# Optimization experiments

Hardware: AMD Instinct MI355X
Metric: run time of the kernel (lower is better)

## Reference

```python
import jax, jax.numpy as jnp
import numpy as np

T, B, IN, H = 512, 64, 512, 1024

def setup_inputs() -> dict:
    key = jax.random.key(0)
    ks = jax.random.split(key, 9)
    s_w = 1.0 / np.sqrt(H + IN)  # torch Linear default init scale
    inp = {"x": jax.random.normal(ks[0], (T, B, IN), dtype=jnp.float32)}
    for name, k in zip(["f", "i", "c", "o"], ks[1:5]):
        inp["W" + name] = jax.random.uniform(k, (H, H + IN), dtype=jnp.float32, minval=-s_w, maxval=s_w)
    for name, k in zip(["f", "i", "c", "o"], ks[5:9]):
        inp["b" + name] = jax.random.uniform(k, (H,), dtype=jnp.float32, minval=-s_w, maxval=s_w)
    return inp

def reference(x, Wf, bf, Wi, bi, Wc, bc, Wo, bo):
    # x: [T, B, IN]; initial h, c are zeros (h=None, c=None path in torch code)
    Bsz = x.shape[1]
    h0 = jnp.zeros((Bsz, H), dtype=x.dtype)
    c0 = jnp.zeros((Bsz, H), dtype=x.dtype)

    def step(carry, x_t):
        h, c = carry
        hx = jnp.concatenate([h, x_t], axis=-1)          # [B, H+IN]
        f = jax.nn.sigmoid(hx @ Wf.T + bf)
        i = jax.nn.sigmoid(hx @ Wi.T + bi)
        c_hat = jnp.tanh(hx @ Wc.T + bc)
        new_c = f * c + i * c_hat
        o = jax.nn.sigmoid(hx @ Wo.T + bo)
        new_h = o * jnp.tanh(new_c)
        return (new_h, new_c), new_h

    _, hs = jax.lax.scan(step, (h0, c0), x)              # hs: [T, B, H]
    return hs
```

## Files before the change

kernel.cpp:

```cpp
#include <hip/hip_runtime.h>
#include <hip/hip_bf16.h>
#include <stdint.h>

#define T_STEPS 512
#define BATCH   64
#define IN_DIM  512
#define H_DIM   1024
#define KDIM    1536
#define NWG     256
#define NTHREADS 256

#define WLDS_OFF 0
#define WLDS_BYTES (24*4*64*16)
#define HA_OFF   98304
#define XA_OFF   131072
#define SMZ_OFF  147456
#define LDS_TOTAL 151616

#define WS_SYNC 0
#define WS_HB   32768
#define WS_XB   294912
#define WS_WPK  33849344

typedef float  f32x4  __attribute__((ext_vector_type(4)));
typedef short  short8 __attribute__((ext_vector_type(8)));
typedef int    int4v  __attribute__((ext_vector_type(4)));
typedef __bf16 bf16x8 __attribute__((ext_vector_type(8)));

__device__ __forceinline__ short f2bf(float f) {
    union { float f; unsigned u; } x; x.f = f;
    unsigned r = (x.u + 0x7fffu + ((x.u >> 16) & 1u)) >> 16;
    return (short)r;
}
__device__ __forceinline__ f32x4 bmfma(short8 a, short8 b, f32x4 c) {
    return __builtin_amdgcn_mfma_f32_16x16x32_bf16(
        __builtin_bit_cast(bf16x8, a), __builtin_bit_cast(bf16x8, b), c, 0, 0, 0);
}

__global__ __launch_bounds__(256) void pack_w_kernel(const float* __restrict__ W,
                                                     short* __restrict__ Wpk, int g) {
    int e = blockIdx.x * 256 + threadIdx.x;
    int j = e / KDIM, k = e - j * KDIM;
    int cb = j >> 4, n = j & 15;
    int ks = k >> 5, grp = (k & 31) >> 3, u = k & 7;
    size_t dst = (((size_t)(cb * 48 + ks) * 4 + g) * 64 + grp * 16 + n) * 8 + u;
    Wpk[dst] = f2bf(W[e]);
}

__global__ __launch_bounds__(256) void xconv_kernel(const float* __restrict__ x,
                                                    short* __restrict__ xb) {
    int e = blockIdx.x * 256 + threadIdx.x;
    int t = e >> 12, rem = e & 4095;
    int brow = rem >> 6, chunk = rem & 63;
    const float* src = x + ((size_t)t * 64 + brow) * IN_DIM + chunk * 8;
    f32x4 v0 = *reinterpret_cast<const f32x4*>(src);
    f32x4 v1 = *reinterpret_cast<const f32x4*>(src + 4);
    short8 o;
    #pragma unroll
    for (int u = 0; u < 4; ++u) { o[u] = f2bf(v0[u]); o[4 + u] = f2bf(v1[u]); }
    int bt = brow >> 4, row = brow & 15, ks = chunk >> 2, grp = chunk & 3;
    size_t dst = (((size_t)t * 4 + bt) * 1024 + ks * 64 + grp * 16 + row) * 8;
    *reinterpret_cast<short8*>(xb + dst) = o;
}

__global__ __launch_bounds__(256) void init_state_kernel(int* sync, int* hb_i) {
    int e = blockIdx.x * 256 + threadIdx.x;
    if (e < 8192) sync[e] = 0;
    if (e < 65536) hb_i[e] = 0;
}

extern "C" __global__ void __launch_bounds__(NTHREADS, 1)
lstm_persistent(const short* __restrict__ Wpk, const short* __restrict__ xb,
                short* __restrict__ hb, float* __restrict__ out,
                const float* __restrict__ bf_, const float* __restrict__ bi_,
                const float* __restrict__ bc_, const float* __restrict__ bo_,
                int* __restrict__ sync)
{
    extern __shared__ char lds[];
    short* Wlds = (short*)(lds + WLDS_OFF);
    short* hA   = (short*)(lds + HA_OFF);
    short* xA   = (short*)(lds + XA_OFF);
    float* smZ  = (float*)(lds + SMZ_OFF);

    const int tid = threadIdx.x, w = tid >> 6, lane = tid & 63;
    const int wg = blockIdx.x;
    const int bt = wg >> 6, cb = wg & 63;
    const int r = lane & 15, hi = lane >> 4;

    const int erow = tid >> 4, ecol = tid & 15;
    const int col_g = cb * 16 + ecol;
    const int row_g = bt * 16 + erow;
    const float bfv = bf_[col_g], biv = bi_[col_g], bcv = bc_[col_g], bov = bo_[col_g];
    float creg = 0.f;

    const int chunkP = col_g >> 3, uP = col_g & 7;
    const int ksP = chunkP >> 2, grpP = chunkP & 3;
    const int pub_off = (ksP * 64 + grpP * 16 + erow) * 8 + uP;

    int* mybarr = sync + bt * 64;

    const short* wgrp = Wpk + (size_t)cb * (48 * 4 * 64 * 8);
    #pragma unroll
    for (int q = 0; q < 24; ++q) {
        int sl = q * 256 + tid;
        *reinterpret_cast<short8*>(Wlds + sl * 8) =
            *reinterpret_cast<const short8*>(wgrp + (size_t)sl * 8);
    }
    const short* wstream = wgrp + (((size_t)24 * 4 + w) * 64 + lane) * 8;

    {
        const short* xtile = xb + ((size_t)0 * 4 + bt) * (1024 * 8);
        #pragma unroll
        for (int q = 0; q < 4; ++q) {
            int sl = q * 256 + tid;
            *reinterpret_cast<short8*>(&xA[sl * 8]) =
                *reinterpret_cast<const short8*>(xtile + (size_t)sl * 8);
        }
    }

    for (int t = 0; t < T_STEPS; ++t) {
        if (t > 0) {
            if (tid == 0) {
                while (__hip_atomic_load(mybarr, __ATOMIC_RELAXED, __HIP_MEMORY_SCOPE_AGENT) < 64 * t)
                    __builtin_amdgcn_s_sleep(1);
            }
        }
        __syncthreads();

        const short* htile = hb + (size_t)(t & 1) * (BATCH * H_DIM) + bt * 16384;
        unsigned long long hlo[8], hhi[8];
        #pragma unroll
        for (int q = 0; q < 8; ++q) {
            const unsigned long long* src = reinterpret_cast<const unsigned long long*>(
                htile + (size_t)(q * 256 + tid) * 8);
            hlo[q] = __hip_atomic_load(src,     __ATOMIC_RELAXED, __HIP_MEMORY_SCOPE_AGENT);
            hhi[q] = __hip_atomic_load(src + 1, __ATOMIC_RELAXED, __HIP_MEMORY_SCOPE_AGENT);
        }
        __builtin_amdgcn_sched_barrier(0);

        f32x4 acc[4];
        #pragma unroll
        for (int c = 0; c < 4; ++c) acc[c] = (f32x4){0.f, 0.f, 0.f, 0.f};
        #pragma unroll
        for (int ksx = 0; ksx < 16; ++ksx) {
            short8 a = *reinterpret_cast<const short8*>(&xA[(ksx * 64 + lane) * 8]);
            short8 b = *reinterpret_cast<const short8*>(wstream + (size_t)(8 + ksx) * 2048);
            acc[ksx & 3] = bmfma(a, b, acc[ksx & 3]);
        }
        __builtin_amdgcn_sched_barrier(0);

        #pragma unroll
        for (int q = 0; q < 8; ++q) {
            unsigned long long tmp[2] = {hlo[q], hhi[q]};
            *reinterpret_cast<int4v*>(&hA[(q * 256 + tid) * 8]) =
                *reinterpret_cast<const int4v*>(tmp);
        }
        __syncthreads();

        #pragma unroll
        for (int ks = 0; ks < 24; ++ks) {
            short8 a = *reinterpret_cast<const short8*>(&hA[(ks * 64 + lane) * 8]);
            short8 b = *reinterpret_cast<const short8*>(Wlds + ((size_t)(ks * 4 + w) * 64 + lane) * 8);
            acc[ks & 3] = bmfma(a, b, acc[ks & 3]);
        }
        #pragma unroll
        for (int ks = 24; ks < 32; ++ks) {
            short8 a = *reinterpret_cast<const short8*>(&hA[(ks * 64 + lane) * 8]);
            short8 b = *reinterpret_cast<const short8*>(wstream + (size_t)(ks - 24) * 2048);
            acc[ks & 3] = bmfma(a, b, acc[ks & 3]);
        }

        f32x4 z4 = (acc[0] + acc[1]) + (acc[2] + acc[3]);
        #pragma unroll
        for (int i = 0; i < 4; ++i)
            smZ[(hi * 4 + i) * 65 + w * 16 + r] = z4[i];
        __syncthreads();

        float zf = smZ[erow * 65 + ecol]      + bfv;
        float zi = smZ[erow * 65 + 16 + ecol] + biv;
        float zc = smZ[erow * 65 + 32 + ecol] + bcv;
        float zo = smZ[erow * 65 + 48 + ecol] + bov;
        float fg  = 1.f / (1.f + __expf(-zf));
        float ig  = 1.f / (1.f + __expf(-zi));
        float cg_ = 2.f / (1.f + __expf(-2.f * zc)) - 1.f;
        float og  = 1.f / (1.f + __expf(-zo));
        creg = fg * creg + ig * cg_;
        float nh = og * (2.f / (1.f + __expf(-2.f * creg)) - 1.f);

        unsigned mybits = (unsigned)(unsigned short)f2bf(nh);
        unsigned pbits  = __shfl_xor(mybits, 1);
        short* hnext_tile = hb + (size_t)((t + 1) & 1) * (BATCH * H_DIM) + bt * 16384;
        if ((tid & 1) == 0) {
            unsigned val = mybits | (pbits << 16);
            __hip_atomic_store(reinterpret_cast<unsigned*>(hnext_tile + pub_off),
                               val, __ATOMIC_RELAXED, __HIP_MEMORY_SCOPE_AGENT);
        }

        __syncthreads();
        if (tid == 0)
            __hip_atomic_fetch_add(mybarr, 1, __ATOMIC_RELAXED, __HIP_MEMORY_SCOPE_AGENT);

        out[(size_t)t * (BATCH * H_DIM) + (size_t)row_g * H_DIM + col_g] = nh;
        if (t + 1 < T_STEPS) {
            const short* xtile = xb + ((size_t)(t + 1) * 4 + bt) * (1024 * 8);
            #pragma unroll
            for (int q = 0; q < 4; ++q) {
                int sl = q * 256 + tid;
                *reinterpret_cast<short8*>(&xA[sl * 8]) =
                    *reinterpret_cast<const short8*>(xtile + (size_t)sl * 8);
            }
        }
    }
}

extern "C" void kernel_launch(void* const* d_in, const int* in_sizes, int n_in,
                              void* d_out, int out_size, void* d_ws, size_t ws_size,
                              hipStream_t stream) {
    const float* x   = (const float*)d_in[0];
    const float* Wf  = (const float*)d_in[1];
    const float* Wi  = (const float*)d_in[2];
    const float* Wc  = (const float*)d_in[3];
    const float* Wo  = (const float*)d_in[4];
    const float* bf_ = (const float*)d_in[5];
    const float* bi_ = (const float*)d_in[6];
    const float* bc_ = (const float*)d_in[7];
    const float* bo_ = (const float*)d_in[8];
    float* out = (float*)d_out;

    char*  ws    = (char*)d_ws;
    int*   syncp = (int*)(ws + WS_SYNC);
    short* hbuf  = (short*)(ws + WS_HB);
    short* xb    = (short*)(ws + WS_XB);
    short* Wpk   = (short*)(ws + WS_WPK);

    hipFuncSetAttribute((const void*)lstm_persistent,
                        hipFuncAttributeMaxDynamicSharedMemorySize, LDS_TOTAL);

    const float* Ws[4] = {Wf, Wi, Wc, Wo};
    for (int g = 0; g < 4; ++g)
        pack_w_kernel<<<(H_DIM * KDIM) / 256, 256, 0, stream>>>(Ws[g], Wpk, g);
    xconv_kernel<<<(T_STEPS * BATCH * IN_DIM) / (256 * 8), 256, 0, stream>>>(x, xb);
    init_state_kernel<<<256, 256, 0, stream>>>(syncp, (int*)hbuf);

    const short* Wpk_c = Wpk; const short* xb_c = xb;
    void* args[] = {(void*)&Wpk_c, (void*)&xb_c, (void*)&hbuf, (void*)&out,
                    (void*)&bf_, (void*)&bi_, (void*)&bc_, (void*)&bo_, (void*)&syncp};
    hipLaunchCooperativeKernel((const void*)lstm_persistent, dim3(NWG), dim3(NTHREADS),
                               args, LDS_TOTAL, stream);
}
```

Before: 1.558 ms.

## Split K dimension across two wave groups with 512 threads per workgroup

Doubles the workgroup to 8 waves and splits the K-reduction of each gate tile between two 4-wave groups. Group 0 uses the LDS-resident weights for h[0:16] and x[0:8], while group 1 streams the remaining weight chunks from global memory. The partial accumulators are combined through a new LDS buffer before the gate nonlinearities. This halves the serial MFMA chain per wave on the critical recurrent path, at the cost of an extra LDS reduction and barrier and an uneven balance between LDS-fed and global-fed groups.

```diff
diff --git a/kernel.cpp b/kernel.cpp
--- a/kernel.cpp
+++ b/kernel.cpp
@@ -8,14 +8,15 @@
 #define H_DIM   1024
 #define KDIM    1536
 #define NWG     256
-#define NTHREADS 256
+#define NTHREADS 512
 
 #define WLDS_OFF 0
 #define WLDS_BYTES (24*4*64*16)
 #define HA_OFF   98304
 #define XA_OFF   131072
-#define SMZ_OFF  147456
-#define LDS_TOTAL 151616
+#define SMP_OFF  147456
+#define SMZ_OFF  151552
+#define LDS_TOTAL 155712
 
 #define WS_SYNC 0
 #define WS_HB   32768
@@ -80,14 +81,17 @@
     short* Wlds = (short*)(lds + WLDS_OFF);
     short* hA   = (short*)(lds + HA_OFF);
     short* xA   = (short*)(lds + XA_OFF);
+    float* smP  = (float*)(lds + SMP_OFF);
     float* smZ  = (float*)(lds + SMZ_OFF);
 
     const int tid = threadIdx.x, w = tid >> 6, lane = tid & 63;
     const int wg = blockIdx.x;
     const int bt = wg >> 6, cb = wg & 63;
     const int r = lane & 15, hi = lane >> 4;
-
-    const int erow = tid >> 4, ecol = tid & 15;
+    const bool grp1 = (w >= 4);
+    const int g = w & 3;
+
+    const int erow = (tid & 255) >> 4, ecol = tid & 15;
     const int col_g = cb * 16 + ecol;
     const int row_g = bt * 16 + erow;
     const float bfv = bf_[col_g], biv = bi_[col_g], bcv = bc_[col_g], bov = bo_[col_g];
@@ -101,19 +105,21 @@
 
     const short* wgrp = Wpk + (size_t)cb * (48 * 4 * 64 * 8);
     #pragma unroll
-    for (int q = 0; q < 24; ++q) {
-        int sl = q * 256 + tid;
-        *reinterpret_cast<short8*>(Wlds + sl * 8) =
-            *reinterpret_cast<const short8*>(wgrp + (size_t)sl * 8);
+    for (int q = 0; q < 12; ++q) {
+        int sl = q * 512 + tid;
+        int e = sl >> 8, within = sl & 255;
+        int gks = (e < 16) ? e : (e + 16);
+        *reinterpret_cast<short8*>(Wlds + (size_t)sl * 8) =
+            *reinterpret_cast<const short8*>(wgrp + ((size_t)(cb == cb ? 0 : 0) + ((size_t)gks * 256 + within)) * 8);
     }
-    const short* wstream = wgrp + (((size_t)24 * 4 + w) * 64 + lane) * 8;
+    const short* wsg = wgrp + ((size_t)g * 64 + lane) * 8;
 
     {
         const short* xtile = xb + ((size_t)0 * 4 + bt) * (1024 * 8);
         #pragma unroll
-        for (int q = 0; q < 4; ++q) {
-            int sl = q * 256 + tid;
-            *reinterpret_cast<short8*>(&xA[sl * 8]) =
+        for (int q = 0; q < 2; ++q) {
+            int sl = q * 512 + tid;
+            *reinterpret_cast<short8*>(&xA[(size_t)sl * 8]) =
                 *reinterpret_cast<const short8*>(xtile + (size_t)sl * 8);
         }
     }
@@ -128,11 +134,11 @@
         __syncthreads();
 
         const short* htile = hb + (size_t)(t & 1) * (BATCH * H_DIM) + bt * 16384;
-        unsigned long long hlo[8], hhi[8];
-        #pragma unroll
-        for (int q = 0; q < 8; ++q) {
+        unsigned long long hlo[4], hhi[4];
+        #pragma unroll
+        for (int q = 0; q < 4; ++q) {
             const unsigned long long* src = reinterpret_cast<const unsigned long long*>(
-                htile + (size_t)(q * 256 + tid) * 8);
+                htile + (size_t)(q * 512 + tid) * 8);
             hlo[q] = __hip_atomic_load(src,     __ATOMIC_RELAXED, __HIP_MEMORY_SCOPE_AGENT);
             hhi[q] = __hip_atomic_load(src + 1, __ATOMIC_RELAXED, __HIP_MEMORY_SCOPE_AGENT);
         }
@@ -141,72 +147,94 @@
         f32x4 acc[4];
         #pragma unroll
         for (int c = 0; c < 4; ++c) acc[c] = (f32x4){0.f, 0.f, 0.f, 0.f};
-        #pragma unroll
-        for (int ksx = 0; ksx < 16; ++ksx) {
-            short8 a = *reinterpret_cast<const short8*>(&xA[(ksx * 64 + lane) * 8]);
-            short8 b = *reinterpret_cast<const short8*>(wstream + (size_t)(8 + ksx) * 2048);
-            acc[ksx & 3] = bmfma(a, b, acc[ksx & 3]);
+        if (!grp1) {
+            #pragma unroll
+            for (int ksx = 0; ksx < 8; ++ksx) {
+                short8 a = *reinterpret_cast<const short8*>(&xA[((ksx) * 64 + lane) * 8]);
+                short8 b = *reinterpret_cast<const short8*>(Wlds + ((size_t)((16 + ksx) * 4 + g) * 64 + lane) * 8);
+                acc[ksx & 3] = bmfma(a, b, acc[ksx & 3]);
+            }
+        } else {
+            #pragma unroll
+            for (int ksx = 8; ksx < 16; ++ksx) {
+                short8 a = *reinterpret_cast<const short8*>(&xA[((ksx) * 64 + lane) * 8]);
+                short8 b = *reinterpret_cast<const short8*>(wsg + (size_t)(32 + ksx) * 2048);
+                acc[ksx & 3] = bmfma(a, b, acc[ksx & 3]);
+            }
         }
         __builtin_amdgcn_sched_barrier(0);
 
         #pragma unroll
-        for (int q = 0; q < 8; ++q) {
+        for (int q = 0; q < 4; ++q) {
             unsigned long long tmp[2] = {hlo[q], hhi[q]};
-            *reinterpret_cast<int4v*>(&hA[(q * 256 + tid) * 8]) =
+            *reinterpret_cast<int4v*>(&hA[(size_t)(q * 512 + tid) * 8]) =
                 *reinterpret_cast<const int4v*>(tmp);
         }
         __syncthreads();
 
-        #pragma unroll
-        for (int ks = 0; ks < 24; ++ks) {
-            short8 a = *reinterpret_cast<const short8*>(&hA[(ks * 64 + lane) * 8]);
-            short8 b = *reinterpret_cast<const short8*>(Wlds + ((size_t)(ks * 4 + w) * 64 + lane) * 8);
-            acc[ks & 3] = bmfma(a, b, acc[ks & 3]);
-        }
-        #pragma unroll
-        for (int ks = 24; ks < 32; ++ks) {
-            short8 a = *reinterpret_cast<const short8*>(&hA[(ks * 64 + lane) * 8]);
-            short8 b = *reinterpret_cast<const short8*>(wstream + (size_t)(ks - 24) * 2048);
-            acc[ks & 3] = bmfma(a, b, acc[ks & 3]);
+        if (!grp1) {
+            #pragma unroll
+            for (int ks = 0; ks < 16; ++ks) {
+                short8 a = *reinterpret_cast<const short8*>(&hA[(ks * 64 + lane) * 8]);
+                short8 b = *reinterpret_cast<const short8*>(Wlds + ((size_t)(ks * 4 + g) * 64 + lane) * 8);
+                acc[ks & 3] = bmfma(a, b, acc[ks & 3]);
+            }
+        } else {
+            #pragma unroll
+            for (int ks = 16; ks < 32; ++ks) {
+                short8 a = *reinterpret_cast<const short8*>(&hA[(ks * 64 + lane) * 8]);
+                short8 b = *reinterpret_cast<const short8*>(wsg + (size_t)ks * 2048);
+                acc[ks & 3] = bmfma(a, b, acc[ks & 3]);
+            }
         }
 
         f32x4 z4 = (acc[0] + acc[1]) + (acc[2] + acc[3]);
-        #pragma unroll
-        for (int i = 0; i < 4; ++i)
-            smZ[(hi * 4 + i) * 65 + w * 16 + r] = z4[i];
-        __syncthreads();
-
-        float zf = smZ[erow * 65 + ecol]      + bfv;
-        float zi = smZ[erow * 65 + 16 + ecol] + biv;
-        float zc = smZ[erow * 65 + 32 + ecol] + bcv;
-        float zo = smZ[erow * 65 + 48 + ecol] + bov;
-        float fg  = 1.f / (1.f + __expf(-zf));
-        float ig  = 1.f / (1.f + __expf(-zi));
-        float cg_ = 2.f / (1.f + __expf(-2.f * zc)) - 1.f;
-        float og  = 1.f / (1.f + __expf(-zo));
-        creg = fg * creg + ig * cg_;
-        float nh = og * (2.f / (1.f + __expf(-2.f * creg)) - 1.f);
-
-        unsigned mybits = (unsigned)(unsigned short)f2bf(nh);
-        unsigned pbits  = __shfl_xor(mybits, 1);
-        short* hnext_tile = hb + (size_t)((t + 1) & 1) * (BATCH * H_DIM) + bt * 16384;
-        if ((tid & 1) == 0) {
-            unsigned val = mybits | (pbits << 16);
-            __hip_atomic_store(reinterpret_cast<unsigned*>(hnext_tile + pub_off),
-                               val, __ATOMIC_RELAXED, __HIP_MEMORY_SCOPE_AGENT);
+        if (grp1)
+            *reinterpret_cast<f32x4*>(smP + ((w - 4) * 64 + lane) * 4) = z4;
+        __syncthreads();
+        if (!grp1) {
+            z4 += *reinterpret_cast<const f32x4*>(smP + (w * 64 + lane) * 4);
+            #pragma unroll
+            for (int i = 0; i < 4; ++i)
+                smZ[(hi * 4 + i) * 65 + w * 16 + r] = z4[i];
+        }
+        __syncthreads();
+
+        float nh = 0.f;
+        if (tid < 256) {
+            float zf = smZ[erow * 65 + ecol]      + bfv;
+            float zi = smZ[erow * 65 + 16 + ecol] + biv;
+            float zc = smZ[erow * 65 + 32 + ecol] + bcv;
+            float zo = smZ[erow * 65 + 48 + ecol] + bov;
+            float fg  = 1.f / (1.f + __expf(-zf));
+            float ig  = 1.f / (1.f + __expf(-zi));
+            float cg_ = 2.f / (1.f + __expf(-2.f * zc)) - 1.f;
+            float og  = 1.f / (1.f + __expf(-zo));
+            creg = fg * creg + ig * cg_;
+            nh = og * (2.f / (1.f + __expf(-2.f * creg)) - 1.f);
+
+            unsigned mybits = (unsigned)(unsigned short)f2bf(nh);
+            unsigned pbits  = __shfl_xor(mybits, 1);
+            short* hnext_tile = hb + (size_t)((t + 1) & 1) * (BATCH * H_DIM) + bt * 16384;
+            if ((tid & 1) == 0) {
+                unsigned val = mybits | (pbits << 16);
+                __hip_atomic_store(reinterpret_cast<unsigned*>(hnext_tile + pub_off),
+                                   val, __ATOMIC_RELAXED, __HIP_MEMORY_SCOPE_AGENT);
+            }
         }
 
         __syncthreads();
         if (tid == 0)
             __hip_atomic_fetch_add(mybarr, 1, __ATOMIC_RELAXED, __HIP_MEMORY_SCOPE_AGENT);
 
-        out[(size_t)t * (BATCH * H_DIM) + (size_t)row_g * H_DIM + col_g] = nh;
+        if (tid < 256)
+            out[(size_t)t * (BATCH * H_DIM) + (size_t)row_g * H_DIM + col_g] = nh;
         if (t + 1 < T_STEPS) {
             const short* xtile = xb + ((size_t)(t + 1) * 4 + bt) * (1024 * 8);
             #pragma unroll
-            for (int q = 0; q < 4; ++q) {
-                int sl = q * 256 + tid;
-                *reinterpret_cast<short8*>(&xA[sl * 8]) =
+            for (int q = 0; q < 2; ++q) {
+                int sl = q * 512 + tid;
+                *reinterpret_cast<short8*>(&xA[(size_t)sl * 8]) =
                     *reinterpret_cast<const short8*>(xtile + (size_t)sl * 8);
             }
         }
```

Result: slower. 2.323 ms (+49.1%).
